# Optimization experiments

Measured on AMD Instinct MI355X. Metric: run time of the kernel, lower is better.

The kernel has to match this reference:

```python
import jax, jax.numpy as jnp
import numpy as np

B, S, E = 2, 2048, 1024
N_HEADS = 16
HEAD_DIM = E // N_HEADS  # 64
ATTN_SCALE = 1.0 / np.sqrt(E)  # NOTE: original scales by 1/sqrt(hidden_dim_phi), not head_dim
ROPE_BASE = 10000.0


def _rope(t):
    # t: (B, H, S, D) with D = HEAD_DIM; interleaved-pair RoPE (torchtune-style)
    d = t.shape[-1]
    s = t.shape[-2]
    inv_freq = 1.0 / (ROPE_BASE ** (jnp.arange(0, d, 2, dtype=jnp.float32) / d))  # (D/2,)
    ang = jnp.arange(s, dtype=jnp.float32)[:, None] * inv_freq[None, :]  # (S, D/2)
    cos, sin = jnp.cos(ang), jnp.sin(ang)  # (S, D/2)
    tp = t.reshape(t.shape[:-1] + (d // 2, 2))
    te, to = tp[..., 0], tp[..., 1]  # (B,H,S,D/2)
    oe = te * cos - to * sin
    oo = te * sin + to * cos
    return jnp.stack([oe, oo], axis=-1).reshape(t.shape)


def setup_inputs() -> dict:
    key = jax.random.key(0)
    ks = jax.random.split(key, 5)
    std = 0.02
    return {
        "x": jax.random.normal(ks[0], (B, S, E), dtype=jnp.float32),
        "W_q": jax.random.normal(ks[1], (E, E), dtype=jnp.float32) * std,
        "W_k": jax.random.normal(ks[2], (E, E), dtype=jnp.float32) * std,
        "W_v": jax.random.normal(ks[3], (E, E), dtype=jnp.float32) * std,
        "W_o": jax.random.normal(ks[4], (E, E), dtype=jnp.float32) * std,
    }


def reference(x, W_q, W_k, W_v, W_o):
    b, s, e = x.shape
    hd = e // N_HEADS
    # projections -> (B, H, S, D)
    def proj(w):
        return (x @ w).reshape(b, s, N_HEADS, hd).transpose(0, 2, 1, 3)
    q = _rope(proj(W_q))
    k = _rope(proj(W_k))
    v = proj(W_v)
    scores = jnp.einsum('bhsd,bhtd->bhst', q, k) * ATTN_SCALE  # (B,H,S,S)
    causal = jnp.triu(jnp.ones((s, s), dtype=bool), k=1)
    scores = jnp.where(causal, -jnp.inf, scores)
    probs = jax.nn.softmax(scores, axis=-1)  # dropout is identity in eval mode
    out = jnp.einsum('bhst,bhtd->bhsd', probs, v)
    out = out.transpose(0, 2, 1, 3).reshape(b, s, e)
    return out @ W_o
```

## Files before the change

kernel.cpp:

```cpp
#include <hip/hip_runtime.h>
#include <hip/hip_bf16.h>

#define S_LEN 2048
#define E_DIM 1024
#define NH 16
#define HD 64
#define ATTN_SCALE 0.03125f
#define QSCALE_L2E 0.045084312f
#define KVB 128

typedef __attribute__((ext_vector_type(8))) short short8;
typedef __attribute__((ext_vector_type(8))) unsigned short ushort8;
typedef __attribute__((ext_vector_type(4))) unsigned short ushort4_t;
typedef __attribute__((ext_vector_type(4))) float f32x4;
typedef __attribute__((ext_vector_type(4))) float f4;
typedef __attribute__((ext_vector_type(2))) unsigned int uint2_t;

__device__ __forceinline__ float bf2f(unsigned short u) {
    unsigned int x = ((unsigned int)u) << 16;
    return __builtin_bit_cast(float, x);
}
__device__ __forceinline__ unsigned short f2bf(float f) {
    unsigned int x = __builtin_bit_cast(unsigned int, f);
    x += 0x7FFFu + ((x >> 16) & 1u);
    return (unsigned short)(x >> 16);
}
__device__ __forceinline__ float exp2_fast(float x) {
    float r;
    asm("v_exp_f32 %0, %1" : "=v"(r) : "v"(x));
    return r;
}
__device__ __forceinline__ void gload16(const unsigned short* g, unsigned short* l) {
    __builtin_amdgcn_global_load_lds(
        (__attribute__((address_space(1))) void*)g,
        (__attribute__((address_space(3))) void*)l, 16, 0, 0);
}

__global__ __launch_bounds__(256) void k_prep(const float* __restrict__ x,
                                              unsigned short* __restrict__ xb,
                                              const float* W0, const float* W1,
                                              const float* W2, const float* W3,
                                              unsigned short* Tqkv,
                                              unsigned short* Twout,
                                              float* __restrict__ cosT,
                                              float* __restrict__ sinT) {
    int bid = blockIdx.x;
    int tid = threadIdx.x;
    if (bid < 2048) {
        size_t i = ((size_t)bid * 256 + tid) * 8;
        f4 a = *(const f4*)(x + i);
        f4 b = *(const f4*)(x + i + 4);
        ushort8 o;
        o[0] = f2bf(a[0]); o[1] = f2bf(a[1]); o[2] = f2bf(a[2]); o[3] = f2bf(a[3]);
        o[4] = f2bf(b[0]); o[5] = f2bf(b[1]); o[6] = f2bf(b[2]); o[7] = f2bf(b[3]);
        *(ushort8*)(xb + i) = o;
    } else if (bid < 2304) {
        int idx = (bid - 2048) * 256 + tid;
        int s = idx >> 5, j = idx & 31;
        float inv = expf(-(float)j * (9.210340371976184f / 32.f));
        float ang = (float)s * inv;
        cosT[idx] = cosf(ang);
        sinT[idx] = sinf(ang);
    } else {
        int t = bid - 2304;
        int bx = (t & 31) * 32, by = ((t >> 5) & 31) * 32, z = t >> 10;
        const float* W; unsigned short* T;
        switch (z) {
            case 0: W = W0; T = Tqkv; break;
            case 1: W = W1; T = Tqkv + 1048576; break;
            case 2: W = W2; T = Tqkv + 2097152; break;
            default: W = W3; T = Twout; break;
        }
        __shared__ float tile[32][33];
        int tx = tid & 31, ty = tid >> 5;
#pragma unroll
        for (int i = 0; i < 4; i++)
            tile[ty + i * 8][tx] = W[(size_t)(by + ty + i * 8) * E_DIM + bx + tx];
        __syncthreads();
#pragma unroll
        for (int i = 0; i < 4; i++)
            T[(size_t)(bx + ty + i * 8) * E_DIM + by + tx] = f2bf(tile[tx][ty + i * 8]);
    }
}

__global__ __launch_bounds__(256, 3)
void k_gemm97(const unsigned short* __restrict__ A,
              const unsigned short* __restrict__ B,
              unsigned short* __restrict__ Qo,
              unsigned short* __restrict__ Ko,
              unsigned short* __restrict__ Vto,
              const float* __restrict__ cosT,
              const float* __restrict__ sinT) {
    constexpr int NBN = 24;
    constexpr int NWG = 32 * NBN;
    __shared__ unsigned short Alds[128 * 64];
    __shared__ unsigned short Blds[128 * 64];
    int tid = threadIdx.x, lane = tid & 63, wid = tid >> 6;
    int l15 = lane & 15, lg = lane >> 4;
    int wr = wid >> 1, wc = wid & 1;
    int orig = blockIdx.y * NBN + blockIdx.x;
    int wg = (orig & 7) * (NWG / 8) + (orig >> 3);
    int bm = wg / NBN, bn = wg % NBN;

    f32x4 acc[4][4] = {};
    for (int k0 = 0; k0 < E_DIM; k0 += 64) {
#pragma unroll
        for (int i = 0; i < 4; i++) {
            int r = wid * 32 + i * 8 + (lane >> 3);
            int cs = (lane & 7) ^ (r & 7);
            gload16(A + (size_t)(bm * 128 + r) * E_DIM + k0 + cs * 8,
                    Alds + (wid * 256 + i * 64) * 8);
        }
#pragma unroll
        for (int i = 0; i < 4; i++) {
            int r = wid * 32 + i * 8 + (lane >> 3);
            int cs = (lane & 7) ^ (r & 7);
            gload16(B + (size_t)(bn * 128 + r) * E_DIM + k0 + cs * 8,
                    Blds + (wid * 256 + i * 64) * 8);
        }
        __syncthreads();
#pragma unroll
        for (int ks = 0; ks < 2; ks++) {
            short8 af[4], bfr[4];
#pragma unroll
            for (int mf = 0; mf < 4; mf++) {
                int r = wr * 64 + mf * 16 + l15;
                int gc = ks * 4 + lg;
                af[mf] = *(const short8*)(Alds + r * 64 + ((gc ^ (r & 7)) << 3));
            }
#pragma unroll
            for (int nf = 0; nf < 4; nf++) {
                int r = wc * 64 + nf * 16 + l15;
                int gc = ks * 4 + lg;
                bfr[nf] = *(const short8*)(Blds + r * 64 + ((gc ^ (r & 7)) << 3));
            }
            __builtin_amdgcn_s_setprio(1);
#pragma unroll
            for (int mf = 0; mf < 4; mf++)
#pragma unroll
                for (int nf = 0; nf < 4; nf++)
                    acc[mf][nf] = __builtin_amdgcn_mfma_f32_16x16x32_bf16(
                        af[mf], bfr[nf], acc[mf][nf], 0, 0, 0);
            __builtin_amdgcn_s_setprio(0);
        }
        __syncthreads();
    }
#pragma unroll
    for (int mf = 0; mf < 4; mf++) {
        int r0 = bm * 128 + wr * 64 + mf * 16 + lg * 4;
#pragma unroll
        for (int nf = 0; nf < 4; nf++) {
            int colg = bn * 128 + wc * 64 + nf * 16 + l15;
            int z = colg >> 10, c1 = colg & 1023;
            if (z == 2) {
                int h = c1 >> 6, d = c1 & 63;
                int bb = r0 >> 11, s = r0 & 2047;
                ushort4_t p;
#pragma unroll
                for (int r = 0; r < 4; r++) p[r] = f2bf(acc[mf][nf][r]);
                *(ushort4_t*)(Vto + (((size_t)((bb * 16 + h) * 64 + d)) << 11) + s) = p;
            } else {
                unsigned short* T = z ? Ko : Qo;
                int dl = c1 & 63, j = dl >> 1;
                float sgn = (dl & 1) ? 1.f : -1.f;
                float scq = z ? 1.f : QSCALE_L2E;
#pragma unroll
                for (int r = 0; r < 4; r++) {
                    int row = r0 + r, s = row & 2047;
                    float c = cosT[s * 32 + j], sn = sinT[s * 32 + j];
                    float v = acc[mf][nf][r];
                    float p = __shfl_xor(v, 1);
                    T[(size_t)row * E_DIM + c1] = f2bf((v * c + sgn * p * sn) * scq);
                }
            }
        }
    }
}

template <int BM, int BN, int NBN>
__global__ __launch_bounds__(256, 3)
void k_gemmo(const unsigned short* __restrict__ A,
             const unsigned short* __restrict__ B,
             float* __restrict__ Fo) {
    constexpr int THREADS = 256;
    constexpr int WM = BM / 2, WN = BN / 2;
    constexpr int FM = WM / 16, FN = WN / 16;
    constexpr int NT = E_DIM / 64;
    constexpr int AR = BM * 8 / THREADS;
    constexpr int BR = BN * 8 / THREADS;
    constexpr int STG = AR + BR;
    constexpr int NWG = (4096 / BM) * NBN;
    __shared__ unsigned short Al[2][BM * 64];
    __shared__ unsigned short Bl[2][BN * 64];
    int tid = threadIdx.x, lane = tid & 63, wid = tid >> 6;
    int l15 = lane & 15, lg = lane >> 4;
    int wr = wid >> 1, wc = wid & 1;
    int orig = blockIdx.y * NBN + blockIdx.x;
    int wg = (orig & 7) * (NWG / 8) + (orig >> 3);
    int bm = wg / NBN, bn = wg % NBN;

    auto stage = [&](int buf, int k0) {
#pragma unroll
        for (int i = 0; i < AR; i++) {
            int r = i * (THREADS / 8) + wid * 8 + (lane >> 3);
            int cs = (lane & 7) ^ (r & 7);
            gload16(A + (size_t)(bm * BM + r) * E_DIM + k0 + cs * 8,
                    &Al[buf][i * (THREADS * 8) + wid * 512]);
        }
#pragma unroll
        for (int i = 0; i < BR; i++) {
            int r = i * (THREADS / 8) + wid * 8 + (lane >> 3);
            int cs = (lane & 7) ^ (r & 7);
            gload16(B + (size_t)(bn * BN + r) * E_DIM + k0 + cs * 8,
                    &Bl[buf][i * (THREADS * 8) + wid * 512]);
        }
    };

    f32x4 acc[FM][FN] = {};
    stage(0, 0);
    for (int t = 0; t < NT; t++) {
        int cur = t & 1;
        if (t + 1 < NT) {
            stage(cur ^ 1, (t + 1) * 64);
            asm volatile("s_waitcnt vmcnt(%0)" :: "n"(STG) : "memory");
        } else {
            asm volatile("s_waitcnt vmcnt(0)" ::: "memory");
        }
        __builtin_amdgcn_s_barrier();
        __builtin_amdgcn_sched_barrier(0);
#pragma unroll
        for (int ks = 0; ks < 2; ks++) {
            short8 af[FM], bfv[FN];
#pragma unroll
            for (int m = 0; m < FM; m++) {
                int r = wr * WM + m * 16 + l15;
                int gc = ks * 4 + lg;
                af[m] = *(const short8*)&Al[cur][r * 64 + ((gc ^ (r & 7)) << 3)];
            }
#pragma unroll
            for (int n = 0; n < FN; n++) {
                int r = wc * WN + n * 16 + l15;
                int gc = ks * 4 + lg;
                bfv[n] = *(const short8*)&Bl[cur][r * 64 + ((gc ^ (r & 7)) << 3)];
            }
            __builtin_amdgcn_s_setprio(1);
#pragma unroll
            for (int m = 0; m < FM; m++)
#pragma unroll
                for (int n = 0; n < FN; n++)
                    acc[m][n] = __builtin_amdgcn_mfma_f32_16x16x32_bf16(
                        af[m], bfv[n], acc[m][n], 0, 0, 0);
            __builtin_amdgcn_s_setprio(0);
        }
        __builtin_amdgcn_s_barrier();
    }
#pragma unroll
    for (int m = 0; m < FM; m++) {
        int r0 = bm * BM + wr * WM + m * 16 + lg * 4;
#pragma unroll
        for (int n = 0; n < FN; n++) {
            int colg = bn * BN + wc * WN + n * 16 + l15;
#pragma unroll
            for (int r = 0; r < 4; r++)
                Fo[(size_t)(r0 + r) * E_DIM + colg] = acc[m][n][r];
        }
    }
}

__global__ __launch_bounds__(256, 3) void k_attn(const unsigned short* __restrict__ Q,
                                                 const unsigned short* __restrict__ K,
                                                 const unsigned short* __restrict__ Vt,
                                                 unsigned short* __restrict__ O) {
    __shared__ unsigned short K_lds[128 * 64];
    __shared__ unsigned short V_lds[64 * 128];
    __shared__ unsigned short P_lds[4][16][136];
    int tid = threadIdx.x, lane = tid & 63, wid = tid >> 6;
    int l15 = lane & 15, lg = lane >> 4;
    int orig = blockIdx.y * 32 + blockIdx.x;
    int xcd = orig & 7, idx = orig >> 3;
    int bh = xcd * 4 + (idx & 3);
    int qt = 31 - ((idx >> 2) & 31);
    int b = bh >> 4, h = bh & 15;
    const size_t base_qk = (size_t)b * S_LEN * E_DIM + (size_t)h * HD;
    const unsigned short* Vbh = Vt + ((size_t)(bh * 64) << 11);

    auto stageK = [&](int kt) {
        const unsigned short* Kb = K + base_qk + (size_t)(kt * KVB) * E_DIM;
#pragma unroll
        for (int i = 0; i < 4; i++) {
            int r = i * 32 + wid * 8 + (lane >> 3);
            int cs = (lane & 7) ^ (r & 7);
            gload16(Kb + (size_t)r * E_DIM + cs * 8, K_lds + i * 2048 + wid * 512);
        }
    };
    auto stageV = [&](int kt) {
#pragma unroll
        for (int i = 0; i < 4; i++) {
            int r = i * 16 + wid * 4 + (lane >> 4);
            int cs = (lane & 15) ^ (r & 7);
            gload16(Vbh + (size_t)r * 2048 + kt * KVB + cs * 8,
                    V_lds + i * 2048 + wid * 512);
        }
    };

    const unsigned short* Qb = Q + base_qk + (size_t)(qt * 64 + wid * 16) * E_DIM;
    short8 bq[2];
#pragma unroll
    for (int s2 = 0; s2 < 2; s2++)
        bq[s2] = *(const short8*)(Qb + (size_t)l15 * E_DIM + s2 * 32 + lg * 8);
    f32x4 acc_o[4] = {};
    float m_i = -1e30f, l_i = 0.f;
    int q_glob = qt * 64 + wid * 16 + l15;
    int nkt = (qt + 2) >> 1;
    stageK(0);
    stageV(0);
    asm volatile("s_waitcnt vmcnt(4)" ::: "memory");
    __builtin_amdgcn_s_barrier();
    __builtin_amdgcn_sched_barrier(0);
    for (int kt = 0; kt < nkt; ++kt) {
        f32x4 acc_s[8] = {};
        __builtin_amdgcn_s_setprio(1);
#pragma unroll
        for (int mf = 0; mf < 8; mf++) {
            int rK = mf * 16 + l15;
#pragma unroll
            for (int s2 = 0; s2 < 2; s2++) {
                int gc = s2 * 4 + lg;
                short8 a = *(const short8*)&K_lds[rK * 64 + ((gc ^ (rK & 7)) << 3)];
                acc_s[mf] = __builtin_amdgcn_mfma_f32_16x16x32_bf16(
                    a, bq[s2], acc_s[mf], 0, 0, 0);
            }
        }
        __builtin_amdgcn_s_setprio(0);
        __builtin_amdgcn_s_barrier();
        if (kt + 1 < nkt) stageK(kt + 1);
        float sv[32];
        float vmax = -1e30f;
        if (kt == nkt - 1) {
#pragma unroll
            for (int mf = 0; mf < 8; mf++)
#pragma unroll
                for (int r = 0; r < 4; r++) {
                    int kg = kt * KVB + mf * 16 + lg * 4 + r;
                    float v = acc_s[mf][r];
                    if (kg > q_glob) v = -1e30f;
                    sv[mf * 4 + r] = v;
                    vmax = fmaxf(vmax, v);
                }
        } else {
#pragma unroll
            for (int mf = 0; mf < 8; mf++)
#pragma unroll
                for (int r = 0; r < 4; r++) {
                    float v = acc_s[mf][r];
                    sv[mf * 4 + r] = v;
                    vmax = fmaxf(vmax, v);
                }
        }
        vmax = fmaxf(vmax, __shfl_xor(vmax, 16));
        vmax = fmaxf(vmax, __shfl_xor(vmax, 32));
        float m_new = fmaxf(m_i, vmax);
        float corr = exp2_fast(m_i - m_new);
        float rowsum = 0.f;
#pragma unroll
        for (int i = 0; i < 32; i++) {
            float p = exp2_fast(sv[i] - m_new);
            sv[i] = p;
            rowsum += p;
        }
        rowsum += __shfl_xor(rowsum, 16);
        rowsum += __shfl_xor(rowsum, 32);
        l_i = l_i * corr + rowsum;
        m_i = m_new;
#pragma unroll
        for (int mf = 0; mf < 8; mf++) {
            unsigned int w0, w1;
            asm("v_cvt_pk_bf16_f32 %0, %1, %2"
                : "=v"(w0) : "v"(sv[mf * 4 + 0]), "v"(sv[mf * 4 + 1]));
            asm("v_cvt_pk_bf16_f32 %0, %1, %2"
                : "=v"(w1) : "v"(sv[mf * 4 + 2]), "v"(sv[mf * 4 + 3]));
            uint2_t w; w[0] = w0; w[1] = w1;
            *(uint2_t*)&P_lds[wid][l15][mf * 16 + lg * 4] = w;
        }
#pragma unroll
        for (int r = 0; r < 4; r++) {
            float c4 = __shfl(corr, lg * 4 + r);
#pragma unroll
            for (int nf = 0; nf < 4; nf++) acc_o[nf][r] *= c4;
        }
        if (kt + 1 < nkt)
            asm volatile("s_waitcnt vmcnt(4)" ::: "memory");
        else
            asm volatile("s_waitcnt vmcnt(0)" ::: "memory");
        __builtin_amdgcn_s_barrier();
        __builtin_amdgcn_sched_barrier(0);
        __builtin_amdgcn_s_setprio(1);
#pragma unroll
        for (int s2 = 0; s2 < 4; s2++) {
            short8 pa = *(const short8*)&P_lds[wid][l15][s2 * 32 + lg * 8];
#pragma unroll
            for (int nf = 0; nf < 4; nf++) {
                int rV = nf * 16 + l15;
                int gc = s2 * 4 + lg;
                short8 bv = *(const short8*)&V_lds[rV * 128 + ((gc ^ (rV & 7)) << 3)];
                acc_o[nf] = __builtin_amdgcn_mfma_f32_16x16x32_bf16(
                    pa, bv, acc_o[nf], 0, 0, 0);
            }
        }
        __builtin_amdgcn_s_setprio(0);
        __builtin_amdgcn_s_barrier();
        if (kt + 1 < nkt) {
            stageV(kt + 1);
            asm volatile("s_waitcnt vmcnt(4)" ::: "memory");
        }
        __builtin_amdgcn_s_barrier();
        __builtin_amdgcn_sched_barrier(0);
    }
    unsigned short* Ob = O + base_qk + (size_t)(qt * 64 + wid * 16) * E_DIM;
#pragma unroll
    for (int r = 0; r < 4; r++) {
        float linv = 1.f / __shfl(l_i, lg * 4 + r);
#pragma unroll
        for (int nf = 0; nf < 4; nf++)
            Ob[(size_t)(lg * 4 + r) * E_DIM + nf * 16 + l15] =
                f2bf(acc_o[nf][r] * linv);
    }
}

extern "C" void kernel_launch(void* const* d_in, const int* in_sizes, int n_in,
                              void* d_out, int out_size, void* d_ws, size_t ws_size,
                              hipStream_t stream) {
    (void)in_sizes; (void)n_in; (void)out_size; (void)ws_size;
    const float* x  = (const float*)d_in[0];
    const float* Wq = (const float*)d_in[1];
    const float* Wk = (const float*)d_in[2];
    const float* Wv = (const float*)d_in[3];
    const float* Wo = (const float*)d_in[4];

    unsigned short* us = (unsigned short*)d_ws;
    unsigned short* xb    = us;
    unsigned short* WqkvT = us + 4194304;
    unsigned short* WoT   = us + 7340032;
    unsigned short* Qb    = us + 8388608;
    unsigned short* Kb    = us + 12582912;
    unsigned short* Vt    = us + 16777216;
    unsigned short* AO    = us + 20971520;
    float* cosT = (float*)((char*)d_ws + 50331648);
    float* sinT = cosT + 65536;

    k_prep<<<6400, 256, 0, stream>>>(x, xb, Wq, Wk, Wv, Wo, WqkvT, WoT, cosT, sinT);
    k_gemm97<<<dim3(24, 32), 256, 0, stream>>>(xb, WqkvT, Qb, Kb, Vt, cosT, sinT);
    k_attn<<<dim3(32, 32), 256, 0, stream>>>(Qb, Kb, Vt, AO);
    k_gemmo<128, 64, 16><<<dim3(16, 32), 256, 0, stream>>>(AO, WoT, (float*)d_out);
}
```

Baseline: 95.75 us.

## Use single-buffered output GEMM and lazy softmax rescaling in attention

```diff
diff --git a/kernel.cpp b/kernel.cpp
--- a/kernel.cpp
+++ b/kernel.cpp
@@ -177,21 +177,14 @@
     }
 }
 
-template <int BM, int BN, int NBN>
 __global__ __launch_bounds__(256, 3)
-void k_gemmo(const unsigned short* __restrict__ A,
-             const unsigned short* __restrict__ B,
-             float* __restrict__ Fo) {
-    constexpr int THREADS = 256;
-    constexpr int WM = BM / 2, WN = BN / 2;
-    constexpr int FM = WM / 16, FN = WN / 16;
-    constexpr int NT = E_DIM / 64;
-    constexpr int AR = BM * 8 / THREADS;
-    constexpr int BR = BN * 8 / THREADS;
-    constexpr int STG = AR + BR;
-    constexpr int NWG = (4096 / BM) * NBN;
-    __shared__ unsigned short Al[2][BM * 64];
-    __shared__ unsigned short Bl[2][BN * 64];
+void k_gemmo97(const unsigned short* __restrict__ A,
+               const unsigned short* __restrict__ B,
+               float* __restrict__ Fo) {
+    constexpr int NBN = 16;
+    constexpr int NWG = 32 * NBN;
+    __shared__ unsigned short Alds[128 * 64];
+    __shared__ unsigned short Blds[64 * 64];
     int tid = threadIdx.x, lane = tid & 63, wid = tid >> 6;
     int l15 = lane & 15, lg = lane >> 4;
     int wr = wid >> 1, wc = wid & 1;
@@ -199,70 +192,60 @@
     int wg = (orig & 7) * (NWG / 8) + (orig >> 3);
     int bm = wg / NBN, bn = wg % NBN;
 
-    auto stage = [&](int buf, int k0) {
-#pragma unroll
-        for (int i = 0; i < AR; i++) {
-            int r = i * (THREADS / 8) + wid * 8 + (lane >> 3);
+    f32x4 acc[4][2] = {};
+    for (int k0 = 0; k0 < E_DIM; k0 += 64) {
+#pragma unroll
+        for (int i = 0; i < 4; i++) {
+            int r = wid * 32 + i * 8 + (lane >> 3);
             int cs = (lane & 7) ^ (r & 7);
-            gload16(A + (size_t)(bm * BM + r) * E_DIM + k0 + cs * 8,
-                    &Al[buf][i * (THREADS * 8) + wid * 512]);
-        }
-#pragma unroll
-        for (int i = 0; i < BR; i++) {
-            int r = i * (THREADS / 8) + wid * 8 + (lane >> 3);
-            int cs = (lane & 7) ^ (r & 7);
-            gload16(B + (size_t)(bn * BN + r) * E_DIM + k0 + cs * 8,
-                    &Bl[buf][i * (THREADS * 8) + wid * 512]);
-        }
-    };
-
-    f32x4 acc[FM][FN] = {};
-    stage(0, 0);
-    for (int t = 0; t < NT; t++) {
-        int cur = t & 1;
-        if (t + 1 < NT) {
-            stage(cur ^ 1, (t + 1) * 64);
-            asm volatile("s_waitcnt vmcnt(%0)" :: "n"(STG) : "memory");
-        } else {
-            asm volatile("s_waitcnt vmcnt(0)" ::: "memory");
-        }
-        __builtin_amdgcn_s_barrier();
-        __builtin_amdgcn_sched_barrier(0);
+            gload16(A + (size_t)(bm * 128 + r) * E_DIM + k0 + cs * 8,
+                    Alds + (wid * 256 + i * 64) * 8);
+        }
+        {
+#pragma unroll
+            for (int i = 0; i < 2; i++) {
+                int r = wid * 16 + i * 8 + (lane >> 3);
+                int cs = (lane & 7) ^ (r & 7);
+                gload16(B + (size_t)(bn * 64 + r) * E_DIM + k0 + cs * 8,
+                        Blds + (wid * 128 + i * 64) * 8);
+            }
+        }
+        __syncthreads();
 #pragma unroll
         for (int ks = 0; ks < 2; ks++) {
-            short8 af[FM], bfv[FN];
-#pragma unroll
-            for (int m = 0; m < FM; m++) {
-                int r = wr * WM + m * 16 + l15;
+            short8 af[4], bfr[2];
+#pragma unroll
+            for (int mf = 0; mf < 4; mf++) {
+                int r = wr * 64 + mf * 16 + l15;
                 int gc = ks * 4 + lg;
-                af[m] = *(const short8*)&Al[cur][r * 64 + ((gc ^ (r & 7)) << 3)];
-            }
-#pragma unroll
-            for (int n = 0; n < FN; n++) {
-                int r = wc * WN + n * 16 + l15;
+                af[mf] = *(const short8*)(Alds + r * 64 + ((gc ^ (r & 7)) << 3));
+            }
+#pragma unroll
+            for (int nf = 0; nf < 2; nf++) {
+                int r = wc * 32 + nf * 16 + l15;
                 int gc = ks * 4 + lg;
-                bfv[n] = *(const short8*)&Bl[cur][r * 64 + ((gc ^ (r & 7)) << 3)];
+                bfr[nf] = *(const short8*)(Blds + r * 64 + ((gc ^ (r & 7)) << 3));
             }
             __builtin_amdgcn_s_setprio(1);
 #pragma unroll
-            for (int m = 0; m < FM; m++)
-#pragma unroll
-                for (int n = 0; n < FN; n++)
-                    acc[m][n] = __builtin_amdgcn_mfma_f32_16x16x32_bf16(
-                        af[m], bfv[n], acc[m][n], 0, 0, 0);
+            for (int mf = 0; mf < 4; mf++)
+#pragma unroll
+                for (int nf = 0; nf < 2; nf++)
+                    acc[mf][nf] = __builtin_amdgcn_mfma_f32_16x16x32_bf16(
+                        af[mf], bfr[nf], acc[mf][nf], 0, 0, 0);
             __builtin_amdgcn_s_setprio(0);
         }
-        __builtin_amdgcn_s_barrier();
-    }
-#pragma unroll
-    for (int m = 0; m < FM; m++) {
-        int r0 = bm * BM + wr * WM + m * 16 + lg * 4;
-#pragma unroll
-        for (int n = 0; n < FN; n++) {
-            int colg = bn * BN + wc * WN + n * 16 + l15;
+        __syncthreads();
+    }
+#pragma unroll
+    for (int mf = 0; mf < 4; mf++) {
+        int r0 = bm * 128 + wr * 64 + mf * 16 + lg * 4;
+#pragma unroll
+        for (int nf = 0; nf < 2; nf++) {
+            int colg = bn * 64 + wc * 32 + nf * 16 + l15;
 #pragma unroll
             for (int r = 0; r < 4; r++)
-                Fo[(size_t)(r0 + r) * E_DIM + colg] = acc[m][n][r];
+                Fo[(size_t)(r0 + r) * E_DIM + colg] = acc[mf][nf][r];
         }
     }
 }
@@ -359,19 +342,28 @@
         }
         vmax = fmaxf(vmax, __shfl_xor(vmax, 16));
         vmax = fmaxf(vmax, __shfl_xor(vmax, 32));
-        float m_new = fmaxf(m_i, vmax);
-        float corr = exp2_fast(m_i - m_new);
+        if (!__all(vmax - m_i <= 8.0f)) {
+            float m_new = fmaxf(m_i, vmax);
+            float corr = exp2_fast(m_i - m_new);
+            l_i *= corr;
+#pragma unroll
+            for (int r = 0; r < 4; r++) {
+                float c4 = __shfl(corr, lg * 4 + r);
+#pragma unroll
+                for (int nf = 0; nf < 4; nf++) acc_o[nf][r] *= c4;
+            }
+            m_i = m_new;
+        }
         float rowsum = 0.f;
 #pragma unroll
         for (int i = 0; i < 32; i++) {
-            float p = exp2_fast(sv[i] - m_new);
+            float p = exp2_fast(sv[i] - m_i);
             sv[i] = p;
             rowsum += p;
         }
         rowsum += __shfl_xor(rowsum, 16);
         rowsum += __shfl_xor(rowsum, 32);
-        l_i = l_i * corr + rowsum;
-        m_i = m_new;
+        l_i += rowsum;
 #pragma unroll
         for (int mf = 0; mf < 8; mf++) {
             unsigned int w0, w1;
@@ -381,12 +373,6 @@
                 : "=v"(w1) : "v"(sv[mf * 4 + 2]), "v"(sv[mf * 4 + 3]));
             uint2_t w; w[0] = w0; w[1] = w1;
             *(uint2_t*)&P_lds[wid][l15][mf * 16 + lg * 4] = w;
-        }
-#pragma unroll
-        for (int r = 0; r < 4; r++) {
-            float c4 = __shfl(corr, lg * 4 + r);
-#pragma unroll
-            for (int nf = 0; nf < 4; nf++) acc_o[nf][r] *= c4;
         }
         if (kt + 1 < nkt)
             asm volatile("s_waitcnt vmcnt(4)" ::: "memory");
@@ -451,5 +437,5 @@
     k_prep<<<6400, 256, 0, stream>>>(x, xb, Wq, Wk, Wv, Wo, WqkvT, WoT, cosT, sinT);
     k_gemm97<<<dim3(24, 32), 256, 0, stream>>>(xb, WqkvT, Qb, Kb, Vt, cosT, sinT);
     k_attn<<<dim3(32, 32), 256, 0, stream>>>(Qb, Kb, Vt, AO);
-    k_gemmo<128, 64, 16><<<dim3(16, 32), 256, 0, stream>>>(AO, WoT, (float*)d_out);
-}
+    k_gemmo97<<<dim3(16, 32), 256, 0, stream>>>(AO, WoT, (float*)d_out);
+}
```

Result: no change. 95.88 us (median of 2 runs) (+0.1%).
